# Kernel tuning notes

Hardware: AMD Instinct MI355X
Metric: run time of the kernel (lower is better)

The kernel has to match this reference:

```python
import jax, jax.numpy as jnp
import numpy as np
from jax import lax
from jax.scipy.special import logsumexp

EPS = 0.005
ITERS = 50
B, N = 8, 2048


def setup_inputs() -> dict:
    key = jax.random.key(0)
    k1, k2 = jax.random.split(key)
    preds = jax.random.normal(k1, (B, N, 3), dtype=jnp.float32)
    gts = jax.random.normal(k2, (B, N, 3), dtype=jnp.float32)
    return {"preds": preds, "gts": gts}


def _emd_loss(preds, gts, eps=EPS, iters=ITERS):
    # Entropic-OT (Sinkhorn) approximation of EMD between equal-size point sets,
    # matching the (eps, iters) iterative matching of the original emdFunction.
    b, n, _ = preds.shape
    # squared-distance cost matrix [B, N, N]
    C = jnp.sum((preds[:, :, None, :] - gts[:, None, :, :]) ** 2, axis=-1)
    log_marg = jnp.full((b, n), -jnp.log(jnp.float32(n)), dtype=C.dtype)  # uniform 1/n
    f0 = jnp.zeros((b, n), dtype=C.dtype)
    g0 = jnp.zeros((b, n), dtype=C.dtype)

    @jax.checkpoint
    def body(carry, _):
        f, g = carry
        # f_i = eps*(log mu_i - logsumexp_j (g_j - C_ij)/eps)
        f = eps * (log_marg - logsumexp((g[:, None, :] - C) / eps, axis=2))
        g = eps * (log_marg - logsumexp((f[:, :, None] - C) / eps, axis=1))
        return (f, g), None

    (f, g), _ = lax.scan(body, (f0, g0), None, length=iters)
    # transport plan P_ij = exp((f_i + g_j - C_ij)/eps); rows sum ~ 1/n
    P = jnp.exp((f[:, :, None] + g[:, None, :] - C) / eps)
    # per-point expected matched squared distance (row marginal = 1/n -> scale by n)
    dis = jnp.float32(n) * jnp.sum(P * C, axis=2)  # [B, N]
    return jnp.mean(dis)


def reference(preds, gts):
    return _emd_loss(preds, gts)
```

## Files before the change

### kernel.cpp

```cpp
#include <hip/hip_runtime.h>


#define BB 8
#define NN 2048
#define NPASS 100
#define ONLINE_PASSES 4
#define RPW 4
#define GRID_BLOCKS 256
#define BLOCKS_PER_BATCH 32
#define TPB 1024
#define CAP 256
#define MARGIN 48.0f

constexpr float EPSV = 0.005f;
constexpr float KS   = EPSV * 0.69314718055994531f;
constexpr float INVK = 1.0f / KS;
constexpr float C1V  = -EPSV * 7.6246189861593985f;
constexpr float C1K  = C1V * INVK;
constexpr float KQ4  = KS * 0.25f;
constexpr float TWOI = 2.0f * INVK;
constexpr float HK   = KS * 0.5f;

__device__ __forceinline__ float fexp2(float x) { return __builtin_amdgcn_exp2f(x); }
__device__ __forceinline__ float flog2(float x) { return __builtin_amdgcn_logf(x); }

__device__ __forceinline__ float cohLoad(const float* p) {
    return __hip_atomic_load(p, __ATOMIC_RELAXED, __HIP_MEMORY_SCOPE_AGENT);
}
__device__ __forceinline__ void cohStore(float* p, float v) {
    __hip_atomic_store(p, v, __ATOMIC_RELAXED, __HIP_MEMORY_SCOPE_AGENT);
}

__device__ __forceinline__ void barrier_sync(int* ctr, int target) {
    __syncthreads();
    if (threadIdx.x == 0) {
        __hip_atomic_fetch_add(ctr, 1, __ATOMIC_RELAXED, __HIP_MEMORY_SCOPE_AGENT);
        while (__hip_atomic_load(ctr, __ATOMIC_RELAXED, __HIP_MEMORY_SCOPE_AGENT) < target) {
            __builtin_amdgcn_s_sleep(1);
        }
    }
    __syncthreads();
}

__global__ void __launch_bounds__(TPB, 4) emd_persist(
    const float* __restrict__ preds, const float* __restrict__ gts,
    float* __restrict__ fpot, float* __restrict__ gpot,
    float* __restrict__ partials, int* __restrict__ bctr, int* __restrict__ gctr,
    float* __restrict__ out)
{
    __shared__ float4 sjall[2 * NN];
    __shared__ float  sa[NN];
    __shared__ float  wred[16];
    __shared__ unsigned short slist[2][64][CAP];

    const int blk  = blockIdx.x;
    const int b    = blk & 7;
    const int rb   = blk >> 3;
    const int wave = threadIdx.x >> 6;
    const int lane = threadIdx.x & 63;
    const int rowL0 = wave * RPW;
    const int row0  = rb * 64 + rowL0;

    const float* pb  = preds + (size_t)b * NN * 3;
    const float* gbp = gts   + (size_t)b * NN * 3;
    float* fb = fpot + (size_t)b * NN;
    float* gb = gpot + (size_t)b * NN;
    int*   bar = bctr + b * 32;

    for (int t = threadIdx.x; t < NN; t += TPB) {
        float gx = gbp[3*t], gy = gbp[3*t+1], gz = gbp[3*t+2];
        float Gx = gx*TWOI, Gy = gy*TWOI, Gz = gz*TWOI;
        sjall[t] = make_float4(Gx, Gy, Gz, -KQ4*(Gx*Gx+Gy*Gy+Gz*Gz));
        float qx = pb[3*t], qy = pb[3*t+1], qz = pb[3*t+2];
        float Qx = qx*TWOI, Qy = qy*TWOI, Qz = qz*TWOI;
        sjall[NN+t] = make_float4(Qx, Qy, Qz, -KQ4*(Qx*Qx+Qy*Qy+Qz*Qz));
    }
    __syncthreads();

    float qxf[RPW], qyf[RPW], qzf[RPW], pcf[RPW];
    float qxg[RPW], qyg[RPW], qzg[RPW], pcg[RPW];
#pragma unroll
    for (int r = 0; r < RPW; ++r) {
        float4 df = sjall[NN + row0 + r];
        qxf[r] = HK*df.x; qyf[r] = HK*df.y; qzf[r] = HK*df.z;
        pcf[r] = C1V - KS*df.w;
        float4 dg = sjall[row0 + r];
        qxg[r] = HK*dg.x; qyg[r] = HK*dg.y; qzg[r] = HK*dg.z;
        pcg[r] = C1V - KS*dg.w;
    }
    float LpF[RPW] = {0,0,0,0}, LpG[RPW] = {0,0,0,0};
    int   cnF[RPW] = {0,0,0,0}, cnG[RPW] = {0,0,0,0};

#pragma unroll 1
    for (int pass = 0; pass < NPASS; ++pass) {
        const int odd = pass & 1;
        const int colOff = odd ? NN : 0;
        const float* pin  = odd ? fb : gb;
        float*       pout = odd ? gb : fb;
        const bool isBuild  = (pass == 4) || (pass == 5);
        const bool isSparse = (pass >= ONLINE_PASSES) && !isBuild;

        float qx[RPW], qy[RPW], qz[RPW], pc[RPW], M[RPW];
#pragma unroll
        for (int r = 0; r < RPW; ++r) {
            qx[r] = odd ? qxg[r] : qxf[r];
            qy[r] = odd ? qyg[r] : qyf[r];
            qz[r] = odd ? qzg[r] : qzf[r];
            pc[r] = odd ? pcg[r] : pcf[r];
            M[r]  = odd ? LpG[r] : LpF[r];
        }

        if (isSparse) {
            float L[RPW];
#pragma unroll
            for (int r = 0; r < RPW; ++r) {
                const int cnt = odd ? cnG[r] : cnF[r];
                const unsigned short* lb = slist[odd][rowL0 + r];
                float s1 = 0.f;
                if (cnt <= CAP) {
#pragma unroll 1
                    for (int k = lane; k < cnt; k += 64) {
                        int j = lb[k];
                        float4 d = sjall[colOff + j];
                        float aw = fmaf(cohLoad(&pin[j]), INVK, d.w);
                        float x  = fmaf(qx[r], d.x, fmaf(qy[r], d.y, fmaf(qz[r], d.z, aw)));
                        s1 += fexp2(fminf(x - M[r], 100.f));
                    }
                } else {
#pragma unroll 1
                    for (int c = 0; c < 32; ++c) {
                        int j = c*64 + lane;
                        float4 d = sjall[colOff + j];
                        float aw = fmaf(cohLoad(&pin[j]), INVK, d.w);
                        float x  = fmaf(qx[r], d.x, fmaf(qy[r], d.y, fmaf(qz[r], d.z, aw)));
                        s1 += fexp2(fminf(x - M[r], 100.f));
                    }
                }
                for (int off = 1; off < 64; off <<= 1) s1 += __shfl_xor(s1, off, 64);
                L[r] = M[r] + flog2(fmaxf(s1, 1e-37f));
            }
#pragma unroll
            for (int r = 0; r < RPW; ++r) {
                if (odd) LpG[r] = L[r]; else LpF[r] = L[r];
                if (lane == 0) cohStore(&pout[row0 + r], pc[r] - KS * L[r]);
            }
        } else {
            for (int t = threadIdx.x; t < NN; t += TPB)
                sa[t] = cohLoad(&pin[t]) * INVK;
            __syncthreads();

            if (pass < ONLINE_PASSES) {
                float m[RPW], s[RPW];
#pragma unroll
                for (int r = 0; r < RPW; ++r) { m[r] = -1e30f; s[r] = 0.f; }
#pragma unroll 2
                for (int c = 0; c < 32; ++c) {
                    float4 d = sjall[colOff + c*64 + lane];
                    float aw = d.w + sa[c*64 + lane];
#pragma unroll
                    for (int r = 0; r < RPW; ++r) {
                        float x  = fmaf(qx[r], d.x, fmaf(qy[r], d.y, fmaf(qz[r], d.z, aw)));
                        float mn = fmaxf(m[r], x);
                        s[r] = fmaf(s[r], fexp2(m[r]-mn), fexp2(x-mn));
                        m[r] = mn;
                    }
                }
#pragma unroll
                for (int r = 0; r < RPW; ++r) {
                    float mm = m[r], sv = s[r];
                    for (int off = 1; off < 64; off <<= 1) {
                        float mo = __shfl_xor(mm, off, 64);
                        float so = __shfl_xor(sv, off, 64);
                        float mn = fmaxf(mm, mo);
                        sv = fmaf(sv, fexp2(mm-mn), so * fexp2(mo-mn));
                        mm = mn;
                    }
                    float L = mm + flog2(fmaxf(sv, 1e-37f));
                    if (odd) LpG[r] = L; else LpF[r] = L;
                    if (lane == 0) cohStore(&pout[row0 + r], pc[r] - KS * L);
                }
            } else {
                float s[RPW]; int cn[RPW];
#pragma unroll
                for (int r = 0; r < RPW; ++r) { s[r] = 0.f; cn[r] = 0; }
#pragma unroll 1
                for (int c = 0; c < 32; ++c) {
                    int j = c*64 + lane;
                    float4 d = sjall[colOff + j];
                    float aw = d.w + sa[j];
#pragma unroll
                    for (int r = 0; r < RPW; ++r) {
                        float x = fmaf(qx[r], d.x, fmaf(qy[r], d.y, fmaf(qz[r], d.z, aw)));
                        s[r] += fexp2(fminf(x - M[r], 100.f));
                        bool pred = (x >= M[r] - MARGIN);
                        unsigned long long mask = __ballot((int)pred);
                        if (pred) {
                            int pos = cn[r] + __popcll(mask & ((1ull << lane) - 1ull));
                            if (pos < CAP) slist[odd][rowL0 + r][pos] = (unsigned short)j;
                        }
                        cn[r] += __popcll(mask);
                    }
                }
#pragma unroll
                for (int r = 0; r < RPW; ++r) {
                    float sv = s[r];
                    for (int off = 1; off < 64; off <<= 1) sv += __shfl_xor(sv, off, 64);
                    float L = M[r] + flog2(fmaxf(sv, 1e-37f));
                    if (odd) { LpG[r] = L; cnG[r] = cn[r]; }
                    else     { LpF[r] = L; cnF[r] = cn[r]; }
                    if (lane == 0) cohStore(&pout[row0 + r], pc[r] - KS * L);
                }
            }
        }
        barrier_sync(bar, BLOCKS_PER_BATCH * (pass + 1));
    }

    {
        float acc[RPW];
#pragma unroll
        for (int r = 0; r < RPW; ++r) acc[r] = 0.f;
#pragma unroll
        for (int r = 0; r < RPW; ++r) {
            const int cnt = cnF[r];
            const unsigned short* lb = slist[0][rowL0 + r];
            const float bb2 = C1K - LpF[r];
            const float pn  = pcf[r] - C1V;
            float aa = 0.f;
            if (cnt <= CAP) {
#pragma unroll 1
                for (int k = lane; k < cnt; k += 64) {
                    int j = lb[k];
                    float4 d = sjall[j];
                    float aw = fmaf(cohLoad(&gb[j]), INVK, d.w);
                    float dot = fmaf(qxf[r], d.x, fmaf(qyf[r], d.y, qzf[r]*d.z));
                    float y   = dot + aw + bb2;
                    float e   = fexp2(fminf(y, 80.f));
                    aa = fmaf(e, fmaf(-KS, dot, pn - KS*d.w), aa);
                }
            } else {
#pragma unroll 1
                for (int c = 0; c < 32; ++c) {
                    int j = c*64 + lane;
                    float4 d = sjall[j];
                    float aw = fmaf(cohLoad(&gb[j]), INVK, d.w);
                    float dot = fmaf(qxf[r], d.x, fmaf(qyf[r], d.y, qzf[r]*d.z));
                    float y   = dot + aw + bb2;
                    float e   = fexp2(fminf(y, 80.f));
                    aa = fmaf(e, fmaf(-KS, dot, pn - KS*d.w), aa);
                }
            }
            acc[r] = aa;
        }
        float tot = acc[0] + acc[1] + acc[2] + acc[3];
        for (int off = 1; off < 64; off <<= 1) tot += __shfl_xor(tot, off, 64);
        if (lane == 0) wred[wave] = tot;
        __syncthreads();
        if (threadIdx.x == 0) {
            float v = 0.f;
            for (int w = 0; w < 16; ++w) v += wred[w];
            cohStore(&partials[blk], v);
        }
    }

    barrier_sync(gctr, GRID_BLOCKS);

    if (blk == 0) {
        float v = (threadIdx.x < GRID_BLOCKS) ? cohLoad(&partials[threadIdx.x]) : 0.f;
        for (int off = 1; off < 64; off <<= 1) v += __shfl_xor(v, off, 64);
        if (lane == 0) wred[wave] = v;
        __syncthreads();
        if (threadIdx.x == 0) {
            float t2 = 0.f;
            for (int w = 0; w < 16; ++w) t2 += wred[w];
            out[0] = t2 * (1.0f / BB);
        }
    }
}

extern "C" void kernel_launch(void* const* d_in, const int* in_sizes, int n_in,
                              void* d_out, int out_size, void* d_ws, size_t ws_size,
                              hipStream_t stream) {
    const float* preds = (const float*)d_in[0];
    const float* gts   = (const float*)d_in[1];
    float* fp       = (float*)d_ws;
    float* gp       = fp + BB * NN;
    float* partials = gp + BB * NN;
    int*   bctr     = (int*)(partials + GRID_BLOCKS);
    int*   gctr     = bctr + BB * 32;
    float* out      = (float*)d_out;

    size_t zbytes = (size_t)(2 * BB * NN + GRID_BLOCKS) * sizeof(float)
                  + (size_t)(BB * 32 + 32) * sizeof(int);
    hipMemsetAsync(d_ws, 0, zbytes, stream);

    emd_persist<<<dim3(GRID_BLOCKS), dim3(TPB), 0, stream>>>(
        preds, gts, fp, gp, partials, bctr, gctr, out);
}
```

Measured before the change: 500.4 us.

## Cache sparse candidate distances and indices in registers for sparse Sinkhorn passes

Splits the pass loop into a dense phase (6 passes) and a sparse phase. After the build passes, each lane precomputes the cost-plus-bias term and packs the candidate column indices into registers, up to 4 per row. The sparse passes then only load the potentials and do the exp, with no LDS list reads or float4 point loads. The four per-row potential stores are merged into two 64-bit atomic stores, and the final reduction reuses the cached terms. This raises register pressure per thread, which matters at 1024 threads per block.

```diff
diff --git a/kernel.cpp b/kernel.cpp
--- a/kernel.cpp
+++ b/kernel.cpp
@@ -4,7 +4,7 @@
 #define BB 8
 #define NN 2048
 #define NPASS 100
-#define ONLINE_PASSES 4
+#define DENSE_PASSES 6
 #define RPW 4
 #define GRID_BLOCKS 256
 #define BLOCKS_PER_BATCH 32
@@ -29,6 +29,13 @@
 }
 __device__ __forceinline__ void cohStore(float* p, float v) {
     __hip_atomic_store(p, v, __ATOMIC_RELAXED, __HIP_MEMORY_SCOPE_AGENT);
+}
+__device__ __forceinline__ void cohStore4(float* p, float a, float b, float c, float d) {
+    union { float f[2]; unsigned long long u; } lo, hi;
+    lo.f[0] = a; lo.f[1] = b; hi.f[0] = c; hi.f[1] = d;
+    unsigned long long* q = (unsigned long long*)p;
+    __hip_atomic_store(q,     lo.u, __ATOMIC_RELAXED, __HIP_MEMORY_SCOPE_AGENT);
+    __hip_atomic_store(q + 1, hi.u, __ATOMIC_RELAXED, __HIP_MEMORY_SCOPE_AGENT);
 }
 
 __device__ __forceinline__ void barrier_sync(int* ctr, int target) {
@@ -92,15 +99,13 @@
     int   cnF[RPW] = {0,0,0,0}, cnG[RPW] = {0,0,0,0};
 
 #pragma unroll 1
-    for (int pass = 0; pass < NPASS; ++pass) {
+    for (int pass = 0; pass < DENSE_PASSES; ++pass) {
         const int odd = pass & 1;
         const int colOff = odd ? NN : 0;
         const float* pin  = odd ? fb : gb;
         float*       pout = odd ? gb : fb;
-        const bool isBuild  = (pass == 4) || (pass == 5);
-        const bool isSparse = (pass >= ONLINE_PASSES) && !isBuild;
-
-        float qx[RPW], qy[RPW], qz[RPW], pc[RPW], M[RPW];
+
+        float qx[RPW], qy[RPW], qz[RPW], pc[RPW], M[RPW], Lr[RPW];
 #pragma unroll
         for (int r = 0; r < RPW; ++r) {
             qx[r] = odd ? qxg[r] : qxf[r];
@@ -110,107 +115,153 @@
             M[r]  = odd ? LpG[r] : LpF[r];
         }
 
-        if (isSparse) {
-            float L[RPW];
+        for (int t = threadIdx.x; t < NN; t += TPB)
+            sa[t] = cohLoad(&pin[t]) * INVK;
+        __syncthreads();
+
+        if (pass < 4) {
+            float m[RPW], s[RPW];
+#pragma unroll
+            for (int r = 0; r < RPW; ++r) { m[r] = -1e30f; s[r] = 0.f; }
+#pragma unroll 2
+            for (int c = 0; c < 32; ++c) {
+                float4 d = sjall[colOff + c*64 + lane];
+                float aw = d.w + sa[c*64 + lane];
+#pragma unroll
+                for (int r = 0; r < RPW; ++r) {
+                    float x  = fmaf(qx[r], d.x, fmaf(qy[r], d.y, fmaf(qz[r], d.z, aw)));
+                    float mn = fmaxf(m[r], x);
+                    s[r] = fmaf(s[r], fexp2(m[r]-mn), fexp2(x-mn));
+                    m[r] = mn;
+                }
+            }
 #pragma unroll
             for (int r = 0; r < RPW; ++r) {
-                const int cnt = odd ? cnG[r] : cnF[r];
-                const unsigned short* lb = slist[odd][rowL0 + r];
-                float s1 = 0.f;
-                if (cnt <= CAP) {
-#pragma unroll 1
-                    for (int k = lane; k < cnt; k += 64) {
-                        int j = lb[k];
-                        float4 d = sjall[colOff + j];
-                        float aw = fmaf(cohLoad(&pin[j]), INVK, d.w);
-                        float x  = fmaf(qx[r], d.x, fmaf(qy[r], d.y, fmaf(qz[r], d.z, aw)));
-                        s1 += fexp2(fminf(x - M[r], 100.f));
+                float mm = m[r], sv = s[r];
+                for (int off = 1; off < 64; off <<= 1) {
+                    float mo = __shfl_xor(mm, off, 64);
+                    float so = __shfl_xor(sv, off, 64);
+                    float mn = fmaxf(mm, mo);
+                    sv = fmaf(sv, fexp2(mm-mn), so * fexp2(mo-mn));
+                    mm = mn;
+                }
+                float L = mm + flog2(fmaxf(sv, 1e-37f));
+                Lr[r] = L;
+                if (odd) LpG[r] = L; else LpF[r] = L;
+            }
+        } else {
+            float s[RPW]; int cn[RPW];
+#pragma unroll
+            for (int r = 0; r < RPW; ++r) { s[r] = 0.f; cn[r] = 0; }
+#pragma unroll 1
+            for (int c = 0; c < 32; ++c) {
+                int j = c*64 + lane;
+                float4 d = sjall[colOff + j];
+                float aw = d.w + sa[j];
+#pragma unroll
+                for (int r = 0; r < RPW; ++r) {
+                    float x = fmaf(qx[r], d.x, fmaf(qy[r], d.y, fmaf(qz[r], d.z, aw)));
+                    s[r] += fexp2(fminf(x - M[r], 100.f));
+                    bool pred = (x >= M[r] - MARGIN);
+                    unsigned long long mask = __ballot((int)pred);
+                    if (pred) {
+                        int pos = cn[r] + __popcll(mask & ((1ull << lane) - 1ull));
+                        if (pos < CAP) slist[odd][rowL0 + r][pos] = (unsigned short)j;
                     }
-                } else {
-#pragma unroll 1
-                    for (int c = 0; c < 32; ++c) {
-                        int j = c*64 + lane;
-                        float4 d = sjall[colOff + j];
-                        float aw = fmaf(cohLoad(&pin[j]), INVK, d.w);
-                        float x  = fmaf(qx[r], d.x, fmaf(qy[r], d.y, fmaf(qz[r], d.z, aw)));
-                        s1 += fexp2(fminf(x - M[r], 100.f));
-                    }
-                }
-                for (int off = 1; off < 64; off <<= 1) s1 += __shfl_xor(s1, off, 64);
-                L[r] = M[r] + flog2(fmaxf(s1, 1e-37f));
+                    cn[r] += __popcll(mask);
+                }
             }
 #pragma unroll
             for (int r = 0; r < RPW; ++r) {
-                if (odd) LpG[r] = L[r]; else LpF[r] = L[r];
-                if (lane == 0) cohStore(&pout[row0 + r], pc[r] - KS * L[r]);
-            }
-        } else {
-            for (int t = threadIdx.x; t < NN; t += TPB)
-                sa[t] = cohLoad(&pin[t]) * INVK;
-            __syncthreads();
-
-            if (pass < ONLINE_PASSES) {
-                float m[RPW], s[RPW];
-#pragma unroll
-                for (int r = 0; r < RPW; ++r) { m[r] = -1e30f; s[r] = 0.f; }
-#pragma unroll 2
-                for (int c = 0; c < 32; ++c) {
-                    float4 d = sjall[colOff + c*64 + lane];
-                    float aw = d.w + sa[c*64 + lane];
-#pragma unroll
-                    for (int r = 0; r < RPW; ++r) {
-                        float x  = fmaf(qx[r], d.x, fmaf(qy[r], d.y, fmaf(qz[r], d.z, aw)));
-                        float mn = fmaxf(m[r], x);
-                        s[r] = fmaf(s[r], fexp2(m[r]-mn), fexp2(x-mn));
-                        m[r] = mn;
-                    }
-                }
-#pragma unroll
-                for (int r = 0; r < RPW; ++r) {
-                    float mm = m[r], sv = s[r];
-                    for (int off = 1; off < 64; off <<= 1) {
-                        float mo = __shfl_xor(mm, off, 64);
-                        float so = __shfl_xor(sv, off, 64);
-                        float mn = fmaxf(mm, mo);
-                        sv = fmaf(sv, fexp2(mm-mn), so * fexp2(mo-mn));
-                        mm = mn;
-                    }
-                    float L = mm + flog2(fmaxf(sv, 1e-37f));
-                    if (odd) LpG[r] = L; else LpF[r] = L;
-                    if (lane == 0) cohStore(&pout[row0 + r], pc[r] - KS * L);
+                float sv = s[r];
+                for (int off = 1; off < 64; off <<= 1) sv += __shfl_xor(sv, off, 64);
+                float L = M[r] + flog2(fmaxf(sv, 1e-37f));
+                Lr[r] = L;
+                if (odd) { LpG[r] = L; cnG[r] = cn[r]; }
+                else     { LpF[r] = L; cnF[r] = cn[r]; }
+            }
+        }
+        if (lane == 0)
+            cohStore4(&pout[row0], pc[0]-KS*Lr[0], pc[1]-KS*Lr[1],
+                                   pc[2]-KS*Lr[2], pc[3]-KS*Lr[3]);
+        barrier_sync(bar, BLOCKS_PER_BATCH * (pass + 1));
+    }
+
+    float XF[RPW][4], XG[RPW][4];
+    unsigned JF[RPW][2], JG[RPW][2];
+    int fbm = 0;
+#pragma unroll
+    for (int r = 0; r < RPW; ++r) {
+        if (cnF[r] > CAP) fbm |= (1 << r);
+        if (cnG[r] > CAP) fbm |= (16 << r);
+        const int cF = cnF[r] < CAP ? cnF[r] : CAP;
+        const int cG = cnG[r] < CAP ? cnG[r] : CAP;
+#pragma unroll
+        for (int c = 0; c < 4; ++c) {
+            const int k = c*64 + lane;
+            int jF = (k < cF) ? (int)slist[0][rowL0 + r][k] : 0;
+            float4 dF = sjall[jF];
+            float xF = fmaf(qxf[r], dF.x, fmaf(qyf[r], dF.y, fmaf(qzf[r], dF.z, dF.w)));
+            XF[r][c] = (k < cF) ? xF : -1e30f;
+            int jG = (k < cG) ? (int)slist[1][rowL0 + r][k] : 0;
+            float4 dG = sjall[NN + jG];
+            float xG = fmaf(qxg[r], dG.x, fmaf(qyg[r], dG.y, fmaf(qzg[r], dG.z, dG.w)));
+            XG[r][c] = (k < cG) ? xG : -1e30f;
+            if ((c & 1) == 0) { JF[r][c>>1] = (unsigned)jF; JG[r][c>>1] = (unsigned)jG; }
+            else              { JF[r][c>>1] |= (unsigned)jF << 16; JG[r][c>>1] |= (unsigned)jG << 16; }
+        }
+    }
+
+#pragma unroll 1
+    for (int pass = DENSE_PASSES; pass < NPASS; ++pass) {
+        const int odd = pass & 1;
+        const int colOff = odd ? NN : 0;
+        const float* pin  = odd ? fb : gb;
+        float*       pout = odd ? gb : fb;
+
+        float L[RPW];
+#pragma unroll
+        for (int r = 0; r < RPW; ++r) {
+            const float Mr = odd ? LpG[r] : LpF[r];
+            const bool  fbk = ((fbm >> (odd ? 4 + r : r)) & 1) != 0;
+            float s1 = 0.f;
+            if (!fbk) {
+                float p[4], Xv[4];
+#pragma unroll
+                for (int c = 0; c < 4; ++c) {
+                    unsigned pk = odd ? JG[r][c>>1] : JF[r][c>>1];
+                    int j = (int)((pk >> ((c & 1) * 16)) & 0xffffu);
+                    p[c]  = cohLoad(&pin[j]);
+                    Xv[c] = odd ? XG[r][c] : XF[r][c];
+                }
+#pragma unroll
+                for (int c = 0; c < 4; ++c) {
+                    float x = fmaf(p[c], INVK, Xv[c]);
+                    s1 += fexp2(fminf(x - Mr, 100.f));
                 }
             } else {
-                float s[RPW]; int cn[RPW];
-#pragma unroll
-                for (int r = 0; r < RPW; ++r) { s[r] = 0.f; cn[r] = 0; }
+                float4 dm = sjall[(odd ? 0 : NN) + row0 + r];
+                float qxr = HK*dm.x, qyr = HK*dm.y, qzr = HK*dm.z;
 #pragma unroll 1
                 for (int c = 0; c < 32; ++c) {
                     int j = c*64 + lane;
                     float4 d = sjall[colOff + j];
-                    float aw = d.w + sa[j];
-#pragma unroll
-                    for (int r = 0; r < RPW; ++r) {
-                        float x = fmaf(qx[r], d.x, fmaf(qy[r], d.y, fmaf(qz[r], d.z, aw)));
-                        s[r] += fexp2(fminf(x - M[r], 100.f));
-                        bool pred = (x >= M[r] - MARGIN);
-                        unsigned long long mask = __ballot((int)pred);
-                        if (pred) {
-                            int pos = cn[r] + __popcll(mask & ((1ull << lane) - 1ull));
-                            if (pos < CAP) slist[odd][rowL0 + r][pos] = (unsigned short)j;
-                        }
-                        cn[r] += __popcll(mask);
-                    }
-                }
-#pragma unroll
-                for (int r = 0; r < RPW; ++r) {
-                    float sv = s[r];
-                    for (int off = 1; off < 64; off <<= 1) sv += __shfl_xor(sv, off, 64);
-                    float L = M[r] + flog2(fmaxf(sv, 1e-37f));
-                    if (odd) { LpG[r] = L; cnG[r] = cn[r]; }
-                    else     { LpF[r] = L; cnF[r] = cn[r]; }
-                    if (lane == 0) cohStore(&pout[row0 + r], pc[r] - KS * L);
-                }
-            }
+                    float aw = fmaf(cohLoad(&pin[j]), INVK, d.w);
+                    float x  = fmaf(qxr, d.x, fmaf(qyr, d.y, fmaf(qzr, d.z, aw)));
+                    s1 += fexp2(fminf(x - Mr, 100.f));
+                }
+            }
+            for (int off = 1; off < 64; off <<= 1) s1 += __shfl_xor(s1, off, 64);
+            L[r] = Mr + flog2(fmaxf(s1, 1e-37f));
+        }
+#pragma unroll
+        for (int r = 0; r < RPW; ++r) { if (odd) LpG[r] = L[r]; else LpF[r] = L[r]; }
+        {
+            float o0 = (odd ? pcg[0] : pcf[0]) - KS*L[0];
+            float o1 = (odd ? pcg[1] : pcf[1]) - KS*L[1];
+            float o2 = (odd ? pcg[2] : pcf[2]) - KS*L[2];
+            float o3 = (odd ? pcg[3] : pcf[3]) - KS*L[3];
+            if (lane == 0) cohStore4(&pout[row0], o0, o1, o2, o3);
         }
         barrier_sync(bar, BLOCKS_PER_BATCH * (pass + 1));
     }
@@ -218,32 +269,30 @@
     {
         float acc[RPW];
 #pragma unroll
-        for (int r = 0; r < RPW; ++r) acc[r] = 0.f;
-#pragma unroll
         for (int r = 0; r < RPW; ++r) {
-            const int cnt = cnF[r];
-            const unsigned short* lb = slist[0][rowL0 + r];
             const float bb2 = C1K - LpF[r];
             const float pn  = pcf[r] - C1V;
             float aa = 0.f;
-            if (cnt <= CAP) {
-#pragma unroll 1
-                for (int k = lane; k < cnt; k += 64) {
-                    int j = lb[k];
-                    float4 d = sjall[j];
-                    float aw = fmaf(cohLoad(&gb[j]), INVK, d.w);
-                    float dot = fmaf(qxf[r], d.x, fmaf(qyf[r], d.y, qzf[r]*d.z));
-                    float y   = dot + aw + bb2;
+            if (((fbm >> r) & 1) == 0) {
+#pragma unroll
+                for (int c = 0; c < 4; ++c) {
+                    unsigned pk = JF[r][c>>1];
+                    int j = (int)((pk >> ((c & 1) * 16)) & 0xffffu);
+                    float D   = XF[r][c];
+                    float pot = cohLoad(&gb[j]);
+                    float y   = fmaf(pot, INVK, D) + bb2;
                     float e   = fexp2(fminf(y, 80.f));
-                    aa = fmaf(e, fmaf(-KS, dot, pn - KS*d.w), aa);
+                    aa = fmaf(e, fmaf(-KS, D, pn), aa);
                 }
             } else {
+                float4 dm = sjall[NN + row0 + r];
+                float qxr = HK*dm.x, qyr = HK*dm.y, qzr = HK*dm.z;
 #pragma unroll 1
                 for (int c = 0; c < 32; ++c) {
                     int j = c*64 + lane;
                     float4 d = sjall[j];
                     float aw = fmaf(cohLoad(&gb[j]), INVK, d.w);
-                    float dot = fmaf(qxf[r], d.x, fmaf(qyf[r], d.y, qzf[r]*d.z));
+                    float dot = fmaf(qxr, d.x, fmaf(qyr, d.y, qzr*d.z));
                     float y   = dot + aw + bb2;
                     float e   = fexp2(fminf(y, 80.f));
                     aa = fmaf(e, fmaf(-KS, dot, pn - KS*d.w), aa);
@@ -291,7 +340,7 @@
 
     size_t zbytes = (size_t)(2 * BB * NN + GRID_BLOCKS) * sizeof(float)
                   + (size_t)(BB * 32 + 32) * sizeof(int);
-    hipMemsetAsync(d_ws, 0, zbytes, stream);
+    (void)hipMemsetAsync(d_ws, 0, zbytes, stream);
 
     emd_persist<<<dim3(GRID_BLOCKS), dim3(TPB), 0, stream>>>(
         preds, gts, fp, gp, partials, bctr, gctr, out);
```

New measurement: 716.0 us. 1.43x slower.
